# Performance work log

Measured on AMD Instinct MI355X. Metric: run time of the kernel, lower is better.

Reference implementation:

```python
import jax, jax.numpy as jnp
import numpy as np

B, T, D, H = 2, 2048, 2048, 16
HD = D // H


def setup_inputs() -> dict:
    key = jax.random.key(0)
    ks = jax.random.split(key, 6)
    s = 1.0 / np.sqrt(D)
    return {
        "x": jax.random.normal(ks[0], (B, T, D), dtype=jnp.float32),
        "Wq": jax.random.normal(ks[1], (D, D), dtype=jnp.float32) * s,
        "Wk": jax.random.normal(ks[2], (D, D), dtype=jnp.float32) * s,
        "Wv": jax.random.normal(ks[3], (D, D), dtype=jnp.float32) * s,
        "Wo": jax.random.normal(ks[4], (D, D), dtype=jnp.float32) * s,
        "bo": jnp.zeros((D,), dtype=jnp.float32),
    }


def reference(x, Wq, Wk, Wv, Wo, bo):
    b, t, d = x.shape
    # projections (torch Linear: x @ W.T)
    q = (x @ Wq.T).reshape(b, t, H, HD).transpose(0, 2, 1, 3)  # [B,H,T,HD]
    k = (x @ Wk.T).reshape(b, t, H, HD).transpose(0, 2, 1, 3)
    v = (x @ Wv.T).reshape(b, t, H, HD).transpose(0, 2, 1, 3)
    scores = jnp.einsum('bhid,bhjd->bhij', q, k) / np.sqrt(HD)  # [B,H,T,T]
    causal = jnp.tril(jnp.ones((t, t), dtype=bool))
    scores = jnp.where(causal[None, None], scores, -jnp.inf)
    attn = jax.nn.softmax(scores, axis=-1)
    out = jnp.einsum('bhij,bhjd->bhid', attn, v)  # [B,H,T,HD]
    out = out.transpose(0, 2, 1, 3).reshape(b, t, d)
    return out @ Wo.T + bo
```

## Files before the change

### kernel.cpp

```cpp
#include <hip/hip_runtime.h>
#include <hip/hip_bf16.h>

#define T_ 2048
#define D_ 2048
#define H_ 16
#define HD_ 128

typedef __hip_bfloat16 bf16;
using bf16x8 = __attribute__((ext_vector_type(8))) short;
using f32x4  = __attribute__((ext_vector_type(4))) float;

#define GLL16(g, l) __builtin_amdgcn_global_load_lds( \
    (const __attribute__((address_space(1))) void*)(g), \
    (__attribute__((address_space(3))) void*)(l), 16, 0, 0)

__device__ __forceinline__ f32x4 mfma16(bf16x8 a, bf16x8 b, f32x4 c) {
    return __builtin_amdgcn_mfma_f32_16x16x32_bf16(a, b, c, 0, 0, 0);
}

__global__ __launch_bounds__(256) void cast6(
    const float* __restrict__ s0, const float* __restrict__ s1,
    const float* __restrict__ s2, const float* __restrict__ s3,
    const float* __restrict__ s4, const float* __restrict__ s5,
    bf16* __restrict__ dst)
{
    int z = blockIdx.y;
    const float* s = (z == 0) ? s0 : (z == 1) ? s1 : (z == 2) ? s2
                   : (z == 3) ? s3 : (z == 4) ? s4 : s5;
    long i = ((long)blockIdx.x * 256 + threadIdx.x) * 8;
    float4 a = *(const float4*)(s + i);
    float4 b = *(const float4*)(s + i + 4);
    union { bf16 h[8]; int4 v; } u;
    u.h[0] = __float2bfloat16(a.x); u.h[1] = __float2bfloat16(a.y);
    u.h[2] = __float2bfloat16(a.z); u.h[3] = __float2bfloat16(a.w);
    u.h[4] = __float2bfloat16(b.x); u.h[5] = __float2bfloat16(b.y);
    u.h[6] = __float2bfloat16(b.z); u.h[7] = __float2bfloat16(b.w);
    *(int4*)(dst + (long)z * 4194304 + i) = u.v;
}

__global__ __launch_bounds__(256) void gemm_qkv(
    const bf16* __restrict__ xb,
    const bf16* __restrict__ wq, const bf16* __restrict__ wk, const bf16* __restrict__ wv,
    bf16* __restrict__ Qo, bf16* __restrict__ Ko, bf16* __restrict__ Vo)
{
    __shared__ bf16 As[128*32];
    __shared__ bf16 Bs[128*32];
    int z = blockIdx.z;
    const bf16* W = (z == 0) ? wq : (z == 1) ? wk : wv;
    bf16* out = (z == 0) ? Qo : (z == 1) ? Ko : Vo;
    int bn = blockIdx.x, bm = blockIdx.y;
    int tid = threadIdx.x, lane = tid & 63, w = tid >> 6;
    int wm = w >> 1, wn = w & 1;
    const bf16* Abase = xb + (long)bm * 128 * D_;
    const bf16* Bbase = W  + (long)bn * 128 * D_;
    int srow = w*16 + (lane >> 2);
    int scol = (lane & 3) * 8;

    f32x4 acc[4][4];
    #pragma unroll
    for (int i = 0; i < 4; ++i)
        #pragma unroll
        for (int j = 0; j < 4; ++j) acc[i][j] = f32x4{0.f,0.f,0.f,0.f};

    for (int kt = 0; kt < D_/32; ++kt) {
        const bf16* Ag = Abase + kt*32;
        const bf16* Bg = Bbase + kt*32;
        GLL16(Ag + (long)srow*D_ + scol,        As + w*512);
        GLL16(Ag + (long)(srow+64)*D_ + scol,   As + 2048 + w*512);
        GLL16(Bg + (long)srow*D_ + scol,        Bs + w*512);
        GLL16(Bg + (long)(srow+64)*D_ + scol,   Bs + 2048 + w*512);
        __syncthreads();
        bf16x8 af[4], bfr[4];
        #pragma unroll
        for (int mt = 0; mt < 4; ++mt)
            af[mt] = *(const bf16x8*)&As[(wm*64 + mt*16 + (lane & 15))*32 + (lane >> 4)*8];
        #pragma unroll
        for (int nt = 0; nt < 4; ++nt)
            bfr[nt] = *(const bf16x8*)&Bs[(wn*64 + nt*16 + (lane & 15))*32 + (lane >> 4)*8];
        #pragma unroll
        for (int mt = 0; mt < 4; ++mt)
            #pragma unroll
            for (int nt = 0; nt < 4; ++nt)
                acc[mt][nt] = mfma16(af[mt], bfr[nt], acc[mt][nt]);
        __syncthreads();
    }
    int mlo = bm*128 + wm*64;
    int nlo = bn*128 + wn*64;
    #pragma unroll
    for (int mt = 0; mt < 4; ++mt) {
        #pragma unroll
        for (int nt = 0; nt < 4; ++nt) {
            int n = nlo + nt*16 + (lane & 15);
            int h = n >> 7, hd = n & 127;
            #pragma unroll
            for (int r = 0; r < 4; ++r) {
                int m = mlo + mt*16 + (lane >> 4)*4 + r;
                int b = m >> 11, t = m & 2047;
                if (z == 2)
                    out[(((long)(b*H_ + h))*HD_ + hd)*T_ + t] = __float2bfloat16(acc[mt][nt][r]);
                else
                    out[(((long)(b*H_ + h))*T_ + t)*HD_ + hd] = __float2bfloat16(acc[mt][nt][r]);
            }
        }
    }
}

__global__ __launch_bounds__(256) void attn(
    const bf16* __restrict__ Qm, const bf16* __restrict__ Km, const bf16* __restrict__ Vm,
    bf16* __restrict__ Om)
{
    __shared__ bf16 Ks[64*136];
    __shared__ bf16 Vt[128*72];
    __shared__ bf16 Ps[128*72];
    int bm = 15 - (blockIdx.x >> 5);
    int bh = blockIdx.x & 31;
    int tid = threadIdx.x, lane = tid & 63, w = tid >> 6;
    const float c1 = 0.12754012780914427f;
    const float c2 = 23.083120654223414f;
    const bf16* Qb = Qm + (long)bh*T_*HD_;
    const bf16* Kb = Km + (long)bh*T_*HD_;
    const bf16* Vb = Vm + (long)bh*HD_*T_;
    int m0 = bm*128 + w*32;

    bf16x8 qf[2][4];
    #pragma unroll
    for (int mt = 0; mt < 2; ++mt)
        #pragma unroll
        for (int ks = 0; ks < 4; ++ks)
            qf[mt][ks] = *(const bf16x8*)(Qb + (long)(m0 + mt*16 + (lane & 15))*HD_ + ks*32 + (lane >> 4)*8);

    bf16x8 onesB;
    {
        short v1 = ((lane & 15) == 0) ? (short)0x3F80 : (short)0;
        #pragma unroll
        for (int jj = 0; jj < 8; ++jj) onesB[jj] = v1;
    }

    f32x4 oacc[2][8];
    f32x4 lacc[2];
    #pragma unroll
    for (int mt = 0; mt < 2; ++mt) {
        lacc[mt] = f32x4{0.f,0.f,0.f,0.f};
        #pragma unroll
        for (int dt = 0; dt < 8; ++dt) oacc[mt][dt] = f32x4{0.f,0.f,0.f,0.f};
    }

    int krow = (tid >> 4);
    int kcg  = tid & 15;
    int vrow = lane >> 3;
    int vcol = (lane & 7) * 8;
    int njt = 2*bm + 2;

    bf16x8 kreg[4], vreg[4];
    #pragma unroll
    for (int i = 0; i < 4; ++i) {
        kreg[i] = *(const bf16x8*)(Kb + (long)(i*16 + krow)*HD_ + kcg*8);
        vreg[i] = *(const bf16x8*)(Vb + (long)(w*32 + i*8 + vrow)*T_ + vcol);
    }

    for (int j = 0; j < njt; ++j) {
        int j0 = j*64;
        __syncthreads();
        #pragma unroll
        for (int i = 0; i < 4; ++i)
            *(bf16x8*)&Ks[(i*16 + krow)*136 + kcg*8] = kreg[i];
        #pragma unroll
        for (int i = 0; i < 4; ++i)
            *(bf16x8*)&Vt[(w*32 + i*8 + vrow)*72 + vcol] = vreg[i];
        __syncthreads();

        if (j + 1 < njt) {
            int jn0 = j0 + 64;
            #pragma unroll
            for (int i = 0; i < 4; ++i) {
                kreg[i] = *(const bf16x8*)(Kb + (long)(jn0 + i*16 + krow)*HD_ + kcg*8);
                vreg[i] = *(const bf16x8*)(Vb + (long)(w*32 + i*8 + vrow)*T_ + jn0 + vcol);
            }
        }

        bool anyv  = (j0 <= m0 + 31);
        if (anyv) {
            bool bmask = (j0 + 63 > m0);
            f32x4 s[2][4];
            #pragma unroll
            for (int mt = 0; mt < 2; ++mt)
                #pragma unroll
                for (int nt = 0; nt < 4; ++nt) s[mt][nt] = f32x4{0.f,0.f,0.f,0.f};
            #pragma unroll
            for (int ks = 0; ks < 4; ++ks) {
                bf16x8 kf[4];
                #pragma unroll
                for (int nt = 0; nt < 4; ++nt)
                    kf[nt] = *(const bf16x8*)&Ks[(nt*16 + (lane & 15))*136 + ks*32 + (lane >> 4)*8];
                #pragma unroll
                for (int mt = 0; mt < 2; ++mt)
                    #pragma unroll
                    for (int nt = 0; nt < 4; ++nt)
                        s[mt][nt] = mfma16(qf[mt][ks], kf[nt], s[mt][nt]);
            }
            #pragma unroll
            for (int mt = 0; mt < 2; ++mt) {
                int prow = w*32 + mt*16 + (lane >> 4)*4;
                #pragma unroll
                for (int nt = 0; nt < 4; ++nt) {
                    int n = j0 + nt*16 + (lane & 15);
                    #pragma unroll
                    for (int r = 0; r < 4; ++r) {
                        float x = fmaf(s[mt][nt][r], c1, -c2);
                        if (bmask) {
                            int mg = m0 + mt*16 + (lane >> 4)*4 + r;
                            x = (n <= mg) ? x : -1e30f;
                        }
                        float p = exp2f(x);
                        Ps[(prow + r)*72 + nt*16 + (lane & 15)] = __float2bfloat16(p);
                    }
                }
            }
            #pragma unroll
            for (int kn = 0; kn < 2; ++kn) {
                bf16x8 pf[2], vf[8];
                #pragma unroll
                for (int mt = 0; mt < 2; ++mt)
                    pf[mt] = *(const bf16x8*)&Ps[(w*32 + mt*16 + (lane & 15))*72 + kn*32 + (lane >> 4)*8];
                #pragma unroll
                for (int dt = 0; dt < 8; ++dt)
                    vf[dt] = *(const bf16x8*)&Vt[(dt*16 + (lane & 15))*72 + kn*32 + (lane >> 4)*8];
                #pragma unroll
                for (int mt = 0; mt < 2; ++mt)
                    lacc[mt] = mfma16(pf[mt], onesB, lacc[mt]);
                #pragma unroll
                for (int mt = 0; mt < 2; ++mt)
                    #pragma unroll
                    for (int dt = 0; dt < 8; ++dt)
                        oacc[mt][dt] = mfma16(pf[mt], vf[dt], oacc[mt][dt]);
            }
        }
    }
    int b = bh >> 4, h = bh & 15;
    #pragma unroll
    for (int mt = 0; mt < 2; ++mt) {
        #pragma unroll
        for (int r = 0; r < 4; ++r) {
            float l = __shfl(lacc[mt][r], lane & 48, 64);
            float inv = 1.f / l;
            int t = m0 + mt*16 + (lane >> 4)*4 + r;
            #pragma unroll
            for (int dt = 0; dt < 8; ++dt) {
                int d = dt*16 + (lane & 15);
                Om[((long)(b*T_ + t))*D_ + h*HD_ + d] = __float2bfloat16(oacc[mt][dt][r] * inv);
            }
        }
    }
}

__global__ __launch_bounds__(256) void gemm_out(
    const bf16* __restrict__ Ab, const bf16* __restrict__ Wob,
    const float* __restrict__ bo, float* __restrict__ out)
{
    __shared__ bf16 As[128*32];
    __shared__ bf16 Bs[128*32];
    int bn = blockIdx.x, bm = blockIdx.y;
    int tid = threadIdx.x, lane = tid & 63, w = tid >> 6;
    int wm = w >> 1, wn = w & 1;
    const bf16* Abase = Ab  + (long)bm * 128 * D_;
    const bf16* Bbase = Wob + (long)bn * 128 * D_;
    int srow = w*16 + (lane >> 2);
    int scol = (lane & 3) * 8;

    f32x4 acc[4][4];
    #pragma unroll
    for (int i = 0; i < 4; ++i)
        #pragma unroll
        for (int j = 0; j < 4; ++j) acc[i][j] = f32x4{0.f,0.f,0.f,0.f};

    for (int kt = 0; kt < D_/32; ++kt) {
        const bf16* Ag = Abase + kt*32;
        const bf16* Bg = Bbase + kt*32;
        GLL16(Ag + (long)srow*D_ + scol,        As + w*512);
        GLL16(Ag + (long)(srow+64)*D_ + scol,   As + 2048 + w*512);
        GLL16(Bg + (long)srow*D_ + scol,        Bs + w*512);
        GLL16(Bg + (long)(srow+64)*D_ + scol,   Bs + 2048 + w*512);
        __syncthreads();
        bf16x8 af[4], bfr[4];
        #pragma unroll
        for (int mt = 0; mt < 4; ++mt)
            af[mt] = *(const bf16x8*)&As[(wm*64 + mt*16 + (lane & 15))*32 + (lane >> 4)*8];
        #pragma unroll
        for (int nt = 0; nt < 4; ++nt)
            bfr[nt] = *(const bf16x8*)&Bs[(wn*64 + nt*16 + (lane & 15))*32 + (lane >> 4)*8];
        #pragma unroll
        for (int mt = 0; mt < 4; ++mt)
            #pragma unroll
            for (int nt = 0; nt < 4; ++nt)
                acc[mt][nt] = mfma16(af[mt], bfr[nt], acc[mt][nt]);
        __syncthreads();
    }
    int mlo = bm*128 + wm*64;
    int nlo = bn*128 + wn*64;
    #pragma unroll
    for (int mt = 0; mt < 4; ++mt) {
        #pragma unroll
        for (int nt = 0; nt < 4; ++nt) {
            int n = nlo + nt*16 + (lane & 15);
            float bias = bo[n];
            #pragma unroll
            for (int r = 0; r < 4; ++r) {
                int m = mlo + mt*16 + (lane >> 4)*4 + r;
                out[(long)m*D_ + n] = acc[mt][nt][r] + bias;
            }
        }
    }
}

extern "C" void kernel_launch(void* const* d_in, const int* in_sizes, int n_in,
                              void* d_out, int out_size, void* d_ws, size_t ws_size,
                              hipStream_t stream) {
    const float* x  = (const float*)d_in[0];
    const float* Wq = (const float*)d_in[1];
    const float* Wk = (const float*)d_in[2];
    const float* Wv = (const float*)d_in[3];
    const float* Wo = (const float*)d_in[4];
    const float* bo = (const float*)d_in[5];
    float* out = (float*)d_out;

    bf16* ws  = (bf16*)d_ws;
    bf16* xb  = ws;
    bf16* wqb = ws + 8388608L;
    bf16* wkb = ws + 12582912L;
    bf16* wvb = ws + 16777216L;
    bf16* wob = ws + 20971520L;
    bf16* Qb  = ws + 25165824L;
    bf16* Kb  = ws + 33554432L;
    bf16* Vb  = ws + 41943040L;
    bf16* Ob  = xb;

    cast6<<<dim3(2048, 6), 256, 0, stream>>>(x, x + 4194304L, Wq, Wk, Wv, Wo, ws);
    gemm_qkv<<<dim3(16, 32, 3), 256, 0, stream>>>(xb, wqb, wkb, wvb, Qb, Kb, Vb);
    attn<<<512, 256, 0, stream>>>(Qb, Kb, Vb, Ob);
    gemm_out<<<dim3(16, 32), 256, 0, stream>>>(Ob, wob, bo, out);
}
```

Baseline: 408.5 us.

## Split long causal attention rows into two KV halves and vectorize V-transpose stores

The attention kernel now splits each of the eight longest query-row blocks into two halves over the key range. Each half writes unnormalized partial outputs and row sums to the workspace, and a new combine kernel adds the two halves and normalizes them. This is meant to even out the causal load imbalance and raise parallelism from 512 to 768 blocks, at the cost of an extra launch and partial-output traffic rounded to bf16. Separately, the transposed V store in the QKV GEMM is vectorized into 4-element writes.

```diff
diff --git a/kernel.cpp b/kernel.cpp
--- a/kernel.cpp
+++ b/kernel.cpp
@@ -86,20 +86,34 @@
     }
     int mlo = bm*128 + wm*64;
     int nlo = bn*128 + wn*64;
-    #pragma unroll
-    for (int mt = 0; mt < 4; ++mt) {
-        #pragma unroll
-        for (int nt = 0; nt < 4; ++nt) {
-            int n = nlo + nt*16 + (lane & 15);
-            int h = n >> 7, hd = n & 127;
-            #pragma unroll
-            for (int r = 0; r < 4; ++r) {
-                int m = mlo + mt*16 + (lane >> 4)*4 + r;
-                int b = m >> 11, t = m & 2047;
-                if (z == 2)
-                    out[(((long)(b*H_ + h))*HD_ + hd)*T_ + t] = __float2bfloat16(acc[mt][nt][r]);
-                else
+    if (z == 2) {
+        #pragma unroll
+        for (int mt = 0; mt < 4; ++mt) {
+            int m0p = mlo + mt*16 + (lane >> 4)*4;
+            int b = m0p >> 11, t0 = m0p & 2047;
+            #pragma unroll
+            for (int nt = 0; nt < 4; ++nt) {
+                int n = nlo + nt*16 + (lane & 15);
+                int h = n >> 7, hd = n & 127;
+                union { bf16 h4[4]; short4 v; } u;
+                #pragma unroll
+                for (int r = 0; r < 4; ++r) u.h4[r] = __float2bfloat16(acc[mt][nt][r]);
+                *(short4*)&out[(((long)(b*H_ + h))*HD_ + hd)*T_ + t0] = u.v;
+            }
+        }
+    } else {
+        #pragma unroll
+        for (int mt = 0; mt < 4; ++mt) {
+            #pragma unroll
+            for (int nt = 0; nt < 4; ++nt) {
+                int n = nlo + nt*16 + (lane & 15);
+                int h = n >> 7, hd = n & 127;
+                #pragma unroll
+                for (int r = 0; r < 4; ++r) {
+                    int m = mlo + mt*16 + (lane >> 4)*4 + r;
+                    int b = m >> 11, t = m & 2047;
                     out[(((long)(b*H_ + h))*T_ + t)*HD_ + hd] = __float2bfloat16(acc[mt][nt][r]);
+                }
             }
         }
     }
@@ -107,13 +121,28 @@
 
 __global__ __launch_bounds__(256) void attn(
     const bf16* __restrict__ Qm, const bf16* __restrict__ Km, const bf16* __restrict__ Vm,
-    bf16* __restrict__ Om)
+    bf16* __restrict__ Om, bf16* __restrict__ Opart, float* __restrict__ lpart)
 {
     __shared__ bf16 Ks[64*136];
     __shared__ bf16 Vt[128*72];
     __shared__ bf16 Ps[128*72];
-    int bm = 15 - (blockIdx.x >> 5);
-    int bh = blockIdx.x & 31;
+    int bx = blockIdx.x;
+    int bm, bh, j_begin, j_end, slot = -1;
+    if (bx < 512) {
+        bm = 15 - (bx >> 6);
+        int r6 = bx & 63;
+        bh = r6 >> 1;
+        int half = r6 & 1;
+        int nj = bm + 1;
+        j_begin = half ? nj : 0;
+        j_end   = half ? (2*bm + 2) : nj;
+        slot = ((bm - 8)*32 + bh)*2 + half;
+    } else {
+        int c = bx - 512;
+        bm = c >> 5;
+        bh = c & 31;
+        j_begin = 0; j_end = 2*bm + 2;
+    }
     int tid = threadIdx.x, lane = tid & 63, w = tid >> 6;
     const float c1 = 0.12754012780914427f;
     const float c2 = 23.083120654223414f;
@@ -149,16 +178,18 @@
     int kcg  = tid & 15;
     int vrow = lane >> 3;
     int vcol = (lane & 7) * 8;
-    int njt = 2*bm + 2;
 
     bf16x8 kreg[4], vreg[4];
-    #pragma unroll
-    for (int i = 0; i < 4; ++i) {
-        kreg[i] = *(const bf16x8*)(Kb + (long)(i*16 + krow)*HD_ + kcg*8);
-        vreg[i] = *(const bf16x8*)(Vb + (long)(w*32 + i*8 + vrow)*T_ + vcol);
-    }
-
-    for (int j = 0; j < njt; ++j) {
+    {
+        int jb = j_begin*64;
+        #pragma unroll
+        for (int i = 0; i < 4; ++i) {
+            kreg[i] = *(const bf16x8*)(Kb + (long)(jb + i*16 + krow)*HD_ + kcg*8);
+            vreg[i] = *(const bf16x8*)(Vb + (long)(w*32 + i*8 + vrow)*T_ + jb + vcol);
+        }
+    }
+
+    for (int j = j_begin; j < j_end; ++j) {
         int j0 = j*64;
         __syncthreads();
         #pragma unroll
@@ -169,7 +200,7 @@
             *(bf16x8*)&Vt[(w*32 + i*8 + vrow)*72 + vcol] = vreg[i];
         __syncthreads();
 
-        if (j + 1 < njt) {
+        if (j + 1 < j_end) {
             int jn0 = j0 + 64;
             #pragma unroll
             for (int i = 0; i < 4; ++i) {
@@ -236,20 +267,66 @@
             }
         }
     }
+    if (bx < 512) {
+        bf16* Op = Opart + (long)slot * 16384;
+        #pragma unroll
+        for (int mt = 0; mt < 2; ++mt) {
+            #pragma unroll
+            for (int r = 0; r < 4; ++r) {
+                int row = w*32 + mt*16 + (lane >> 4)*4 + r;
+                if ((lane & 15) == 0) lpart[slot*128 + row] = lacc[mt][r];
+                #pragma unroll
+                for (int dt = 0; dt < 8; ++dt)
+                    Op[row*128 + dt*16 + (lane & 15)] = __float2bfloat16(oacc[mt][dt][r]);
+            }
+        }
+    } else {
+        int b = bh >> 4, h = bh & 15;
+        #pragma unroll
+        for (int mt = 0; mt < 2; ++mt) {
+            #pragma unroll
+            for (int r = 0; r < 4; ++r) {
+                float l = __shfl(lacc[mt][r], lane & 48, 64);
+                float inv = 1.f / l;
+                int t = m0 + mt*16 + (lane >> 4)*4 + r;
+                #pragma unroll
+                for (int dt = 0; dt < 8; ++dt) {
+                    int d = dt*16 + (lane & 15);
+                    Om[((long)(b*T_ + t))*D_ + h*HD_ + d] = __float2bfloat16(oacc[mt][dt][r] * inv);
+                }
+            }
+        }
+    }
+}
+
+__global__ __launch_bounds__(256) void combine(
+    const bf16* __restrict__ Opart, const float* __restrict__ lpart,
+    bf16* __restrict__ Om)
+{
+    int blk = blockIdx.x;
+    int sbm = blk >> 5, bh = blk & 31;
+    int bm = 8 + sbm;
+    int slot0 = blk*2, slot1 = blk*2 + 1;
+    int tid = threadIdx.x;
+    int row = tid >> 1;
+    int dh = (tid & 1)*64;
+    const bf16* p0 = Opart + (long)slot0*16384 + row*128 + dh;
+    const bf16* p1 = Opart + (long)slot1*16384 + row*128 + dh;
+    float inv = 1.f / (lpart[slot0*128 + row] + lpart[slot1*128 + row]);
     int b = bh >> 4, h = bh & 15;
-    #pragma unroll
-    for (int mt = 0; mt < 2; ++mt) {
-        #pragma unroll
-        for (int r = 0; r < 4; ++r) {
-            float l = __shfl(lacc[mt][r], lane & 48, 64);
-            float inv = 1.f / l;
-            int t = m0 + mt*16 + (lane >> 4)*4 + r;
-            #pragma unroll
-            for (int dt = 0; dt < 8; ++dt) {
-                int d = dt*16 + (lane & 15);
-                Om[((long)(b*T_ + t))*D_ + h*HD_ + d] = __float2bfloat16(oacc[mt][dt][r] * inv);
-            }
-        }
+    int t = bm*128 + row;
+    bf16* o = Om + ((long)(b*T_ + t))*D_ + h*HD_ + dh;
+    #pragma unroll
+    for (int i = 0; i < 8; ++i) {
+        bf16x8 a = *(const bf16x8*)(p0 + i*8);
+        bf16x8 c = *(const bf16x8*)(p1 + i*8);
+        union { bf16 h8[8]; bf16x8 v; } ua, uc, uo;
+        ua.v = a; uc.v = c;
+        #pragma unroll
+        for (int jj = 0; jj < 8; ++jj)
+            uo.h8[jj] = __float2bfloat16(
+                (__bfloat162float(ua.h8[jj]) + __bfloat162float(uc.h8[jj])) * inv);
+        *(bf16x8*)(o + i*8) = uo.v;
     }
 }
 
@@ -333,9 +410,12 @@
     bf16* Kb  = ws + 33554432L;
     bf16* Vb  = ws + 41943040L;
     bf16* Ob  = xb;
+    bf16*  Opart = wqb;
+    float* lpart = (float*)(ws + 16777216L);
 
     cast6<<<dim3(2048, 6), 256, 0, stream>>>(x, x + 4194304L, Wq, Wk, Wv, Wo, ws);
     gemm_qkv<<<dim3(16, 32, 3), 256, 0, stream>>>(xb, wqb, wkb, wvb, Qb, Kb, Vb);
-    attn<<<512, 256, 0, stream>>>(Qb, Kb, Vb, Ob);
+    attn<<<768, 256, 0, stream>>>(Qb, Kb, Vb, Ob, Opart, lpart);
+    combine<<<256, 256, 0, stream>>>(Opart, lpart, Ob);
     gemm_out<<<dim3(16, 32), 256, 0, stream>>>(Ob, wob, bo, out);
 }
```

Measured after the change: 423.0 us. 3.5% more time.
